# Optimization experiments

Hardware: AMD Instinct MI355X
Metric: run time of the kernel (lower is better)

The kernel has to match this reference:

```python
import jax, jax.numpy as jnp
import numpy as np
from jax import lax

DN = ('NCHW', 'OIHW', 'NCHW')
BN_EPS = 1e-5


def _conv(x, w, pad):
    # pad: list of (lo, hi) for H, W
    return lax.conv_general_dilated(x, w, (1, 1), pad, dimension_numbers=DN)


def _grid_sample_bilinear(img, grid):
    """F.grid_sample(img, grid, align_corners=True, padding_mode='zeros').
    img: [N,C,H,W], grid: [N,Ho,Wo,2] with (x,y) in [-1,1]."""
    N, C, H, W = img.shape
    gx, gy = grid[..., 0], grid[..., 1]
    # align_corners=True mapping to pixel coords
    ix = (gx + 1.0) * 0.5 * (W - 1)
    iy = (gy + 1.0) * 0.5 * (H - 1)
    x0 = jnp.floor(ix)
    y0 = jnp.floor(iy)
    x1 = x0 + 1.0
    y1 = y0 + 1.0
    # bilinear weights
    wa = (x1 - ix) * (y1 - iy)  # top-left (x0,y0)
    wb = (ix - x0) * (y1 - iy)  # top-right (x1,y0)
    wc = (x1 - ix) * (iy - y0)  # bottom-left (x0,y1)
    wd = (ix - x0) * (iy - y0)  # bottom-right (x1,y1)

    imgc = jnp.transpose(img, (0, 2, 3, 1))  # [N,H,W,C]
    b = jnp.arange(N)[:, None, None]

    def gather(xi, yi):
        valid = (xi >= 0) & (xi <= W - 1) & (yi >= 0) & (yi <= H - 1)
        xc = jnp.clip(xi, 0, W - 1).astype(jnp.int32)
        yc = jnp.clip(yi, 0, H - 1).astype(jnp.int32)
        v = imgc[b, yc, xc]  # [N,Ho,Wo,C]
        return v * valid[..., None].astype(img.dtype)

    out = (gather(x0, y0) * wa[..., None] + gather(x1, y0) * wb[..., None]
           + gather(x0, y1) * wc[..., None] + gather(x1, y1) * wd[..., None])
    return jnp.transpose(out, (0, 3, 1, 2))  # [N,C,Ho,Wo]


def setup_inputs() -> dict:
    key = jax.random.key(0)
    ks = jax.random.split(key, 12)
    N, C1, C2 = 8, 512, 256
    H, W = 64, 64
    x1 = jax.random.normal(ks[0], (N, C1, 2 * H, 2 * W), dtype=jnp.float32)
    x2 = jax.random.normal(ks[1], (N, C2, H, W), dtype=jnp.float32)
    w_change = jax.random.normal(ks[2], (C2, C1, 1, 1), dtype=jnp.float32) * 0.02
    b_change = jax.random.normal(ks[3], (C2,), dtype=jnp.float32) * 0.02
    w_cc1 = jax.random.normal(ks[4], (C2, 2 * C2, 1, 1), dtype=jnp.float32) * 0.02
    bn_gamma = 1.0 + 0.1 * jax.random.normal(ks[5], (C2,), dtype=jnp.float32)
    bn_beta = 0.1 * jax.random.normal(ks[6], (C2,), dtype=jnp.float32)
    bn_mean = 0.1 * jax.random.normal(ks[7], (C2,), dtype=jnp.float32)
    bn_var = jax.random.uniform(ks[8], (C2,), dtype=jnp.float32, minval=0.5, maxval=1.5)
    w_cc2 = jax.random.normal(ks[9], (4, C2, 3, 3), dtype=jnp.float32) * 0.02
    return {"x1": x1, "x2": x2, "w_change": w_change, "b_change": b_change,
            "w_cc1": w_cc1, "bn_gamma": bn_gamma, "bn_beta": bn_beta,
            "bn_mean": bn_mean, "bn_var": bn_var, "w_cc2": w_cc2}


def reference(x1, x2, w_change, b_change, w_cc1, bn_gamma, bn_beta, bn_mean, bn_var, w_cc2):
    # MaxPool2d(2,2)
    x1p = lax.reduce_window(x1, -jnp.inf, lax.max, (1, 1, 2, 2), (1, 1, 2, 2), 'VALID')
    # change: 1x1 conv with bias
    x1c = _conv(x1p, w_change, [(0, 0), (0, 0)]) + b_change[None, :, None, None]
    # concat + concat_conv (1x1 conv -> BN(eval) -> ReLU -> 3x3 conv)
    x = jnp.concatenate([x1c, x2], axis=1)
    x = _conv(x, w_cc1, [(0, 0), (0, 0)])
    inv = lax.rsqrt(bn_var + BN_EPS)
    x = (x - bn_mean[None, :, None, None]) * (inv * bn_gamma)[None, :, None, None] + bn_beta[None, :, None, None]
    x = jax.nn.relu(x)
    flow = _conv(x, w_cc2, [(1, 1), (1, 1)])  # [N,4,H,W]
    flow1 = flow[:, :2]
    flow2 = flow[:, 2:]

    N, _, H, W = x1c.shape
    # base grid: [...,0]=x over width, [...,1]=y over height
    xs = jnp.linspace(-1.0, 1.0, W, dtype=x1c.dtype)
    ys = jnp.linspace(-1.0, 1.0, H, dtype=x1c.dtype)
    base = jnp.stack(jnp.meshgrid(xs, ys, indexing='xy'), axis=-1)  # [H,W,2]
    norm = jnp.array([(W - 1) / 2.0, (H - 1) / 2.0], dtype=x1c.dtype)

    grid1 = base[None] + jnp.transpose(flow1, (0, 2, 3, 1)) / norm
    grid2 = base[None] + jnp.transpose(flow2, (0, 2, 3, 1)) / norm

    u1 = _grid_sample_bilinear(x1c, grid1)
    u2 = _grid_sample_bilinear(x2, grid2)
    return u1 + u2
```

## Files before the change

### kernel.cpp

```cpp
#include <hip/hip_runtime.h>
#include <hip/hip_bf16.h>

#define NB 8
#define C1 512
#define C2 256
#define HWSZ 4096
#define BN_EPS 1e-5f
#define P2 264

typedef __hip_bfloat16 bf16;
typedef __hip_bfloat162 bf162;
typedef __attribute__((ext_vector_type(8))) short short8v;
typedef __attribute__((ext_vector_type(4))) float f32x4;

static __device__ inline float b2f(bf16 h) { return __bfloat162float(h); }

static __device__ inline float us2f(unsigned short u) {
  union { unsigned u32; float f; } c; c.u32 = ((unsigned)u) << 16; return c.f;
}

static __device__ inline unsigned short f2bf(float f) {
  union { bf16 h; unsigned short u; } c;
  c.h = __float2bfloat16(f);
  return c.u;
}

static __device__ inline unsigned pack2(float a, float b) {
  union { unsigned u; bf162 h; } pk;
  pk.h = __float22bfloat162_rn(make_float2(a, b));
  return pk.u;
}

static __device__ inline uint2 pack4(float a, float b, float c, float d) {
  union { uint2 u; bf162 h[2]; } pk;
  pk.h[0] = __float22bfloat162_rn(make_float2(a, b));
  pk.h[1] = __float22bfloat162_rn(make_float2(c, d));
  return pk.u;
}

#define SBARQ() asm volatile("s_waitcnt lgkmcnt(0)\n\ts_barrier" ::: "memory")
#define SBAR()  asm volatile("s_barrier" ::: "memory")
#define LGKM0() asm volatile("s_waitcnt lgkmcnt(0)" ::: "memory")

__global__ __launch_bounds__(256) void k0_swizzle(
    const float* __restrict__ wch, const float* __restrict__ wcc1,
    const float* __restrict__ wcc2,
    unsigned short* __restrict__ wchB, unsigned short* __restrict__ wcc1B,
    float* __restrict__ wr) {
  const int t = blockIdx.x * 256 + threadIdx.x;
  if (t < 262144) {
    const int which = t >> 17;
    const int r = t & 131071;
    const int i = r & 7;
    const int lane = (r >> 3) & 63;
    const int ntile = (r >> 9) & 15;
    const int kstep = r >> 13;
    const int ci = kstep * 32 + (lane >> 4) * 8 + i;
    const int co = ntile * 16 + (lane & 15);
    const float* s = which ? wcc1 : wch;
    unsigned short* d = which ? wcc1B : wchB;
    d[r] = f2bf(s[co * 512 + ci]);
  } else if (t < 262144 + 9216) {
    const int r = t - 262144;
    const int f = r / 2304;
    const int rr = r % 2304;
    const int ci = rr / 9;
    const int tt = rr % 9;
    wr[ci * 36 + (tt / 3) * 12 + (tt % 3) * 4 + f] = wcc2[r];
  }
}

__global__ __launch_bounds__(512) void k12_fused(
    const float* __restrict__ x1, const float* __restrict__ x2,
    const unsigned short* __restrict__ wchB, const unsigned short* __restrict__ wcc1B,
    const float* __restrict__ bch,
    const float* __restrict__ gamma, const float* __restrict__ beta,
    const float* __restrict__ mean, const float* __restrict__ var,
    unsigned short* __restrict__ x1c_nhwc, unsigned short* __restrict__ x2_nhwc,
    bf16* __restrict__ xbn) {
  __shared__ unsigned short As[64 * 40];
  __shared__ unsigned short As2[64 * P2];
  const int tid = threadIdx.x;
  const int lane = tid & 63;
  const int wv = tid >> 6;
  const int lrow = lane & 15;
  const int lgrp = lane >> 4;

  const int m0g = blockIdx.x * 64;
  const int n = m0g >> 12;
  const int hw0 = m0g & 4095;
  const int h = hw0 >> 6;

  f32x4 acc[4][2];
#pragma unroll
  for (int mt = 0; mt < 4; ++mt)
#pragma unroll
    for (int nt = 0; nt < 2; ++nt) acc[mt][nt] = (f32x4){0.f, 0.f, 0.f, 0.f};

  const int pmi = tid & 31;
  const int ms = pmi * 2;
  const int ch0 = (tid >> 5) * 2;

  const float* x1p = x1 + (size_t)n * C1 * 16384 + (size_t)(2 * h) * 128 + 2 * ms;

  float4 t0, b0, t1, b1;
#define LOADA(K0_) do { \
    const float* p_ = x1p + (size_t)((K0_) + ch0) * 16384; \
    t0 = *(const float4*)p_;            b0 = *(const float4*)(p_ + 128); \
    t1 = *(const float4*)(p_ + 16384);  b1 = *(const float4*)(p_ + 16384 + 128); \
  } while (0)
#define POOLA(U0_, U1_) do { \
    U0_ = pack2(fmaxf(fmaxf(t0.x, t0.y), fmaxf(b0.x, b0.y)), \
                fmaxf(fmaxf(t1.x, t1.y), fmaxf(b1.x, b1.y))); \
    U1_ = pack2(fmaxf(fmaxf(t0.z, t0.w), fmaxf(b0.z, b0.w)), \
                fmaxf(fmaxf(t1.z, t1.w), fmaxf(b1.z, b1.w))); \
  } while (0)

  unsigned uA0, uA1;
  LOADA(0);
  POOLA(uA0, uA1);
  LOADA(32);

  for (int ks = 0; ks < 16; ++ks) {
    SBARQ();
    *(unsigned*)&As[ms * 40 + ch0] = uA0;
    *(unsigned*)&As[(ms + 1) * 40 + ch0] = uA1;
    LGKM0();
    SBAR();

    unsigned uN0, uN1;
    if (ks < 15) {
      POOLA(uN0, uN1);
      if (ks < 14) LOADA((ks + 2) * 32);
    }

    short8v a[4];
#pragma unroll
    for (int mt = 0; mt < 4; ++mt)
      a[mt] = *(const short8v*)&As[(mt * 16 + lrow) * 40 + lgrp * 8];
#pragma unroll
    for (int nt = 0; nt < 2; ++nt) {
      const int ntile = wv * 2 + nt;
      const short8v b = *(const short8v*)&wchB[(size_t)((ks * 16 + ntile) * 64 + lane) * 8];
#pragma unroll
      for (int mt = 0; mt < 4; ++mt)
        acc[mt][nt] = __builtin_amdgcn_mfma_f32_16x16x32_bf16(a[mt], b, acc[mt][nt], 0, 0, 0);
    }
    if (ks < 15) { uA0 = uN0; uA1 = uN1; }
  }

  const int chB = tid >> 4;
  const int mqB = (tid & 15) * 4;
  float4 cf0 = *(const float4*)&x2[((size_t)(n * C2 + chB)) * HWSZ + hw0 + mqB];
  float4 cf1 = *(const float4*)&x2[((size_t)(n * C2 + 32 + chB)) * HWSZ + hw0 + mqB];

#pragma unroll
  for (int nt = 0; nt < 2; ++nt) {
    const int co = (wv * 2 + nt) * 16 + lrow;
    const float bias = bch[co];
#pragma unroll
    for (int mt = 0; mt < 4; ++mt) {
      const f32x4 v = acc[mt][nt];
      const uint2 pk = pack4(v.x + bias, v.y + bias, v.z + bias, v.w + bias);
      const int mb = mt * 16 + lgrp * 4;
      As2[(mb + 0) * P2 + co] = (unsigned short)(pk.x & 0xffffu);
      As2[(mb + 1) * P2 + co] = (unsigned short)(pk.x >> 16);
      As2[(mb + 2) * P2 + co] = (unsigned short)(pk.y & 0xffffu);
      As2[(mb + 3) * P2 + co] = (unsigned short)(pk.y >> 16);
      acc[mt][nt] = (f32x4){0.f, 0.f, 0.f, 0.f};
    }
  }
  LGKM0();
  SBAR();

  {
    const int mm = tid >> 3;
    const int cg = (tid & 7) * 32;
    const size_t ob = ((size_t)(m0g + mm)) * 256 + cg;
#pragma unroll
    for (int k = 0; k < 4; ++k) {
      const uint4 v = *(const uint4*)&As2[mm * P2 + cg + k * 8];
      *(uint4*)&x1c_nhwc[ob + k * 8] = v;
    }
  }

#pragma unroll
  for (int ks = 0; ks < 8; ++ks) {
    short8v a[4];
#pragma unroll
    for (int mt = 0; mt < 4; ++mt)
      a[mt] = *(const short8v*)&As2[(mt * 16 + lrow) * P2 + ks * 32 + lgrp * 8];
#pragma unroll
    for (int nt = 0; nt < 2; ++nt) {
      const int ntile = wv * 2 + nt;
      const short8v b = *(const short8v*)&wcc1B[(size_t)((ks * 16 + ntile) * 64 + lane) * 8];
#pragma unroll
      for (int mt = 0; mt < 4; ++mt)
        acc[mt][nt] = __builtin_amdgcn_mfma_f32_16x16x32_bf16(a[mt], b, acc[mt][nt], 0, 0, 0);
    }
  }

  for (int ks = 8; ks < 16; ++ks) {
    const unsigned p0 = pack2(cf0.x, cf0.y);
    const unsigned p1 = pack2(cf0.z, cf0.w);
    cf0 = cf1;
    if (ks < 14) {
      cf1 = *(const float4*)&x2[((size_t)(n * C2 + (ks - 6) * 32 + chB)) * HWSZ + hw0 + mqB];
    }
    SBARQ();
    As[(mqB + 0) * 40 + chB] = (unsigned short)(p0 & 0xffffu);
    As[(mqB + 1) * 40 + chB] = (unsigned short)(p0 >> 16);
    As[(mqB + 2) * 40 + chB] = (unsigned short)(p1 & 0xffffu);
    As[(mqB + 3) * 40 + chB] = (unsigned short)(p1 >> 16);
    LGKM0();
    SBAR();

    {
      const int m = tid >> 3;
      const int c4 = (tid & 7) * 4;
      const uint2 v = *(const uint2*)&As[m * 40 + c4];
      *(uint2*)&x2_nhwc[((size_t)(m0g + m)) * 256 + (ks - 8) * 32 + c4] = v;
    }

    short8v a[4];
#pragma unroll
    for (int mt = 0; mt < 4; ++mt)
      a[mt] = *(const short8v*)&As[(mt * 16 + lrow) * 40 + lgrp * 8];
#pragma unroll
    for (int nt = 0; nt < 2; ++nt) {
      const int ntile = wv * 2 + nt;
      const short8v b = *(const short8v*)&wcc1B[(size_t)((ks * 16 + ntile) * 64 + lane) * 8];
#pragma unroll
      for (int mt = 0; mt < 4; ++mt)
        acc[mt][nt] = __builtin_amdgcn_mfma_f32_16x16x32_bf16(a[mt], b, acc[mt][nt], 0, 0, 0);
    }
  }

#pragma unroll
  for (int nt = 0; nt < 2; ++nt) {
    const int co = (wv * 2 + nt) * 16 + lrow;
    const float sc = gamma[co] * rsqrtf(var[co] + BN_EPS);
    const float sh = beta[co] - mean[co] * sc;
#pragma unroll
    for (int mt = 0; mt < 4; ++mt) {
      const f32x4 vv = acc[mt][nt];
      *(uint2*)&xbn[((size_t)(n * C2 + co)) * HWSZ + hw0 + mt * 16 + lgrp * 4] =
          pack4(fmaxf(vv.x * sc + sh, 0.f), fmaxf(vv.y * sc + sh, 0.f),
                fmaxf(vv.z * sc + sh, 0.f), fmaxf(vv.w * sc + sh, 0.f));
    }
  }
#undef LOADA
#undef POOLA
}

__global__ __launch_bounds__(1024) void k34_conv_sample(
    const bf16* __restrict__ xbn, const float* __restrict__ wr,
    const unsigned short* __restrict__ x1c_nhwc,
    const unsigned short* __restrict__ x2_nhwc,
    float* __restrict__ out) {
  __shared__ union {
    struct { float wsm[9216]; float part[16][4][64]; } c;
    float outT[256][65];
  } sh;
  __shared__ float flr[4][64];
  __shared__ int   toff[8][64];
  __shared__ float twt[8][64];

  const int tid = threadIdx.x;
  const int n = blockIdx.x >> 6;
  const int h = blockIdx.x & 63;
  const int wl = tid & 63;
  const int q = tid >> 6;

  for (int idx = tid; idx < 9216; idx += 1024) sh.c.wsm[idx] = wr[idx];
  __syncthreads();

  float acc[4] = {0.f, 0.f, 0.f, 0.f};
  {
    const bf16* base = xbn + ((size_t)(n * C2 + q * 16)) * HWSZ;
    const float* wq = sh.c.wsm + (q * 16) * 36;
    for (int cc = 0; cc < 16; ++cc) {
      const bf16* src = base + (size_t)cc * HWSZ;
      const float* wc = wq + cc * 36;
#pragma unroll
      for (int dy = 0; dy < 3; ++dy) {
        const int y = h + dy - 1;
        if ((unsigned)y >= 64u) continue;
        const float v = b2f(src[y * 64 + wl]);
        float vm = __shfl_up(v, 1);
        float vp = __shfl_down(v, 1);
        if (wl == 0) vm = 0.f;
        if (wl == 63) vp = 0.f;
        const float4 wa = *(const float4*)&wc[dy * 12 + 0];
        const float4 wb = *(const float4*)&wc[dy * 12 + 4];
        const float4 wd = *(const float4*)&wc[dy * 12 + 8];
        acc[0] = fmaf(vm, wa.x, fmaf(v, wb.x, fmaf(vp, wd.x, acc[0])));
        acc[1] = fmaf(vm, wa.y, fmaf(v, wb.y, fmaf(vp, wd.y, acc[1])));
        acc[2] = fmaf(vm, wa.z, fmaf(v, wb.z, fmaf(vp, wd.z, acc[2])));
        acc[3] = fmaf(vm, wa.w, fmaf(v, wb.w, fmaf(vp, wd.w, acc[3])));
      }
    }
  }
  sh.c.part[q][0][wl] = acc[0];
  sh.c.part[q][1][wl] = acc[1];
  sh.c.part[q][2][wl] = acc[2];
  sh.c.part[q][3][wl] = acc[3];
  __syncthreads();
  if (tid < 256) {
    const int f = tid >> 6;
    const int ww = tid & 63;
    float s = 0.f;
#pragma unroll
    for (int qq = 0; qq < 16; ++qq) s += sh.c.part[qq][f][ww];
    flr[f][ww] = s;
  }
  __syncthreads();

  if (tid < 64) {
    const float fxv[2] = {flr[0][tid], flr[2][tid]};
    const float fyv[2] = {flr[1][tid], flr[3][tid]};
#pragma unroll
    for (int s = 0; s < 2; ++s) {
      const float ix = (float)tid + fxv[s], iy = (float)h + fyv[s];
      const float x0f = floorf(ix), y0f = floorf(iy);
      const float fx = ix - x0f, fy = iy - y0f;
      const int x0 = (int)x0f, y0 = (int)y0f, x1i = x0 + 1, y1i = y0 + 1;
      const float vx0 = (x0 >= 0 && x0 < 64) ? 1.f : 0.f;
      const float vx1 = (x1i >= 0 && x1i < 64) ? 1.f : 0.f;
      const float vy0 = (y0 >= 0 && y0 < 64) ? 1.f : 0.f;
      const float vy1 = (y1i >= 0 && y1i < 64) ? 1.f : 0.f;
      const int cx0 = min(max(x0, 0), 63), cx1 = min(max(x1i, 0), 63);
      const int cy0 = min(max(y0, 0), 63), cy1 = min(max(y1i, 0), 63);
      toff[s * 4 + 0][tid] = cy0 * 64 + cx0;
      toff[s * 4 + 1][tid] = cy0 * 64 + cx1;
      toff[s * 4 + 2][tid] = cy1 * 64 + cx0;
      toff[s * 4 + 3][tid] = cy1 * 64 + cx1;
      twt[s * 4 + 0][tid] = (1.f - fx) * (1.f - fy) * vx0 * vy0;
      twt[s * 4 + 1][tid] = fx * (1.f - fy) * vx1 * vy0;
      twt[s * 4 + 2][tid] = (1.f - fx) * fy * vx0 * vy1;
      twt[s * 4 + 3][tid] = fx * fy * vx1 * vy1;
    }
  }
  __syncthreads();

  {
    const unsigned short* pb1 = x1c_nhwc + (size_t)n * HWSZ * 256 + wl * 4;
    const unsigned short* pb2 = x2_nhwc + (size_t)n * HWSZ * 256 + wl * 4;
#pragma unroll
    for (int pp = 0; pp < 4; ++pp) {
      const int p = q * 4 + pp;
      float u0 = 0.f, u1 = 0.f, u2 = 0.f, u3 = 0.f;
#pragma unroll
      for (int t = 0; t < 8; ++t) {
        const int off = toff[t][p];
        const float wt = twt[t][p];
        const unsigned short* rp = (t < 4 ? pb1 : pb2) + (size_t)off * 256;
        const uint2 v = *(const uint2*)rp;
        u0 = fmaf(wt, us2f((unsigned short)(v.x & 0xffffu)), u0);
        u1 = fmaf(wt, us2f((unsigned short)(v.x >> 16)), u1);
        u2 = fmaf(wt, us2f((unsigned short)(v.y & 0xffffu)), u2);
        u3 = fmaf(wt, us2f((unsigned short)(v.y >> 16)), u3);
      }
      sh.outT[wl * 4 + 0][p] = u0;
      sh.outT[wl * 4 + 1][p] = u1;
      sh.outT[wl * 4 + 2][p] = u2;
      sh.outT[wl * 4 + 3][p] = u3;
    }
  }
  __syncthreads();

  {
    const int p = tid & 63;
    const int cg = (tid >> 6) * 16;
    const size_t ob = ((size_t)(n * C2 + cg)) * HWSZ + h * 64 + p;
#pragma unroll
    for (int j = 0; j < 16; ++j) {
      out[ob + (size_t)j * HWSZ] = sh.outT[cg + j][p];
    }
  }
}

extern "C" void kernel_launch(void* const* d_in, const int* in_sizes, int n_in,
                              void* d_out, int out_size, void* d_ws, size_t ws_size,
                              hipStream_t stream) {
  const float* x1      = (const float*)d_in[0];
  const float* x2      = (const float*)d_in[1];
  const float* w_change= (const float*)d_in[2];
  const float* b_change= (const float*)d_in[3];
  const float* w_cc1   = (const float*)d_in[4];
  const float* bn_gamma= (const float*)d_in[5];
  const float* bn_beta = (const float*)d_in[6];
  const float* bn_mean = (const float*)d_in[7];
  const float* bn_var  = (const float*)d_in[8];
  const float* w_cc2   = (const float*)d_in[9];
  float* out = (float*)d_out;

  unsigned short* x1c_nhwc = (unsigned short*)d_ws;
  bf16*           xbn      = (bf16*)((char*)d_ws + (16u << 20));
  unsigned short* x2_nhwc  = (unsigned short*)((char*)d_ws + (32u << 20));
  unsigned short* wchB     = (unsigned short*)((char*)d_ws + (48u << 20));
  unsigned short* wcc1B    = (unsigned short*)((char*)d_ws + (48u << 20) + (256u << 10));
  float*          wr       = (float*)((char*)d_ws + (48u << 20) + (512u << 10));

  k0_swizzle<<<1060, 256, 0, stream>>>(w_change, w_cc1, w_cc2, wchB, wcc1B, wr);
  k12_fused<<<512, 512, 0, stream>>>(x1, x2, wchB, wcc1B, b_change,
                                     bn_gamma, bn_beta, bn_mean, bn_var,
                                     x1c_nhwc, x2_nhwc, xbn);
  k34_conv_sample<<<512, 1024, 0, stream>>>(xbn, wr, x1c_nhwc, x2_nhwc, out);
}
```

Before: 139.5 us.

## Fuse 3x3 flow conv into 1x1 conv kernel via shared-memory staging and atomics

The BN+ReLU output is now kept in shared memory inside the fused 1x1-conv kernel instead of being written to global memory as bf16. The same kernel computes the 3x3 flow convolution for its row and scatters partial sums to the neighbouring rows of a zero-initialized flow buffer with atomicAdd. The sampling kernel then only reads the precomputed flow. This removes a 16 MB intermediate write and read and the weight staging in the last kernel. In exchange it adds float atomics, which make the summation order nondeterministic, and an extra zeroing pass in the prep kernel.

```diff
diff --git a/kernel.cpp b/kernel.cpp
--- a/kernel.cpp
+++ b/kernel.cpp
@@ -13,8 +13,6 @@
 typedef __attribute__((ext_vector_type(8))) short short8v;
 typedef __attribute__((ext_vector_type(4))) float f32x4;
 
-static __device__ inline float b2f(bf16 h) { return __bfloat162float(h); }
-
 static __device__ inline float us2f(unsigned short u) {
   union { unsigned u32; float f; } c; c.u32 = ((unsigned)u) << 16; return c.f;
 }
@@ -42,11 +40,11 @@
 #define SBAR()  asm volatile("s_barrier" ::: "memory")
 #define LGKM0() asm volatile("s_waitcnt lgkmcnt(0)" ::: "memory")
 
-__global__ __launch_bounds__(256) void k0_swizzle(
+__global__ __launch_bounds__(256) void k0_prep(
     const float* __restrict__ wch, const float* __restrict__ wcc1,
     const float* __restrict__ wcc2,
     unsigned short* __restrict__ wchB, unsigned short* __restrict__ wcc1B,
-    float* __restrict__ wr) {
+    float* __restrict__ wr, float* __restrict__ flow) {
   const int t = blockIdx.x * 256 + threadIdx.x;
   if (t < 262144) {
     const int which = t >> 17;
@@ -67,6 +65,8 @@
     const int ci = rr / 9;
     const int tt = rr % 9;
     wr[ci * 36 + (tt / 3) * 12 + (tt % 3) * 4 + f] = wcc2[r];
+  } else if (t < 262144 + 9216 + 131072) {
+    flow[t - 262144 - 9216] = 0.f;
   }
 }
 
@@ -76,8 +76,9 @@
     const float* __restrict__ bch,
     const float* __restrict__ gamma, const float* __restrict__ beta,
     const float* __restrict__ mean, const float* __restrict__ var,
+    const float* __restrict__ wr,
     unsigned short* __restrict__ x1c_nhwc, unsigned short* __restrict__ x2_nhwc,
-    bf16* __restrict__ xbn) {
+    float* __restrict__ flow) {
   __shared__ unsigned short As[64 * 40];
   __shared__ unsigned short As2[64 * P2];
   const int tid = threadIdx.x;
@@ -236,6 +237,7 @@
     }
   }
 
+  SBARQ();
 #pragma unroll
   for (int nt = 0; nt < 2; ++nt) {
     const int co = (wv * 2 + nt) * 16 + lrow;
@@ -244,24 +246,55 @@
 #pragma unroll
     for (int mt = 0; mt < 4; ++mt) {
       const f32x4 vv = acc[mt][nt];
-      *(uint2*)&xbn[((size_t)(n * C2 + co)) * HWSZ + hw0 + mt * 16 + lgrp * 4] =
-          pack4(fmaxf(vv.x * sc + sh, 0.f), fmaxf(vv.y * sc + sh, 0.f),
-                fmaxf(vv.z * sc + sh, 0.f), fmaxf(vv.w * sc + sh, 0.f));
-    }
+      const uint2 pk = pack4(fmaxf(vv.x * sc + sh, 0.f), fmaxf(vv.y * sc + sh, 0.f),
+                             fmaxf(vv.z * sc + sh, 0.f), fmaxf(vv.w * sc + sh, 0.f));
+      const int mb = mt * 16 + lgrp * 4;
+      As2[(mb + 0) * P2 + co] = (unsigned short)(pk.x & 0xffffu);
+      As2[(mb + 1) * P2 + co] = (unsigned short)(pk.x >> 16);
+      As2[(mb + 2) * P2 + co] = (unsigned short)(pk.y & 0xffffu);
+      As2[(mb + 3) * P2 + co] = (unsigned short)(pk.y >> 16);
+    }
+  }
+  LGKM0();
+  SBAR();
+
+  {
+    const int xp = tid & 63;
+    const int fh = tid >> 6;
+    const int f = fh & 3;
+    const int half = fh >> 2;
+    float pm = 0.f, pz = 0.f, pp = 0.f;
+    for (int ci = half * 128; ci < half * 128 + 128; ci += 2) {
+      const float* w0 = wr + ci * 36 + f;
+#pragma unroll
+      for (int dx = 0; dx < 3; ++dx) {
+        const int xs = xp + dx - 1;
+        if ((unsigned)xs >= 64u) continue;
+        const unsigned vv = *(const unsigned*)&As2[xs * P2 + ci];
+        const float v0 = us2f((unsigned short)(vv & 0xffffu));
+        const float v1 = us2f((unsigned short)(vv >> 16));
+        const float* wa = w0 + dx * 4;
+        const float* wb = wa + 36;
+        pm = fmaf(v0, wa[24], fmaf(v1, wb[24], pm));
+        pz = fmaf(v0, wa[12], fmaf(v1, wb[12], pz));
+        pp = fmaf(v0, wa[0],  fmaf(v1, wb[0],  pp));
+      }
+    }
+    float* fb = flow + ((size_t)(n * 4 + f)) * HWSZ + xp;
+    if (h >= 1)  atomicAdd(fb + (h - 1) * 64, pm);
+    atomicAdd(fb + h * 64, pz);
+    if (h <= 62) atomicAdd(fb + (h + 1) * 64, pp);
   }
 #undef LOADA
 #undef POOLA
 }
 
-__global__ __launch_bounds__(1024) void k34_conv_sample(
-    const bf16* __restrict__ xbn, const float* __restrict__ wr,
+__global__ __launch_bounds__(1024) void k4_sample(
+    const float* __restrict__ flow,
     const unsigned short* __restrict__ x1c_nhwc,
     const unsigned short* __restrict__ x2_nhwc,
     float* __restrict__ out) {
-  __shared__ union {
-    struct { float wsm[9216]; float part[16][4][64]; } c;
-    float outT[256][65];
-  } sh;
+  __shared__ float outT[256][65];
   __shared__ float flr[4][64];
   __shared__ int   toff[8][64];
   __shared__ float twt[8][64];
@@ -272,47 +305,9 @@
   const int wl = tid & 63;
   const int q = tid >> 6;
 
-  for (int idx = tid; idx < 9216; idx += 1024) sh.c.wsm[idx] = wr[idx];
-  __syncthreads();
-
-  float acc[4] = {0.f, 0.f, 0.f, 0.f};
-  {
-    const bf16* base = xbn + ((size_t)(n * C2 + q * 16)) * HWSZ;
-    const float* wq = sh.c.wsm + (q * 16) * 36;
-    for (int cc = 0; cc < 16; ++cc) {
-      const bf16* src = base + (size_t)cc * HWSZ;
-      const float* wc = wq + cc * 36;
-#pragma unroll
-      for (int dy = 0; dy < 3; ++dy) {
-        const int y = h + dy - 1;
-        if ((unsigned)y >= 64u) continue;
-        const float v = b2f(src[y * 64 + wl]);
-        float vm = __shfl_up(v, 1);
-        float vp = __shfl_down(v, 1);
-        if (wl == 0) vm = 0.f;
-        if (wl == 63) vp = 0.f;
-        const float4 wa = *(const float4*)&wc[dy * 12 + 0];
-        const float4 wb = *(const float4*)&wc[dy * 12 + 4];
-        const float4 wd = *(const float4*)&wc[dy * 12 + 8];
-        acc[0] = fmaf(vm, wa.x, fmaf(v, wb.x, fmaf(vp, wd.x, acc[0])));
-        acc[1] = fmaf(vm, wa.y, fmaf(v, wb.y, fmaf(vp, wd.y, acc[1])));
-        acc[2] = fmaf(vm, wa.z, fmaf(v, wb.z, fmaf(vp, wd.z, acc[2])));
-        acc[3] = fmaf(vm, wa.w, fmaf(v, wb.w, fmaf(vp, wd.w, acc[3])));
-      }
-    }
-  }
-  sh.c.part[q][0][wl] = acc[0];
-  sh.c.part[q][1][wl] = acc[1];
-  sh.c.part[q][2][wl] = acc[2];
-  sh.c.part[q][3][wl] = acc[3];
-  __syncthreads();
   if (tid < 256) {
-    const int f = tid >> 6;
-    const int ww = tid & 63;
-    float s = 0.f;
-#pragma unroll
-    for (int qq = 0; qq < 16; ++qq) s += sh.c.part[qq][f][ww];
-    flr[f][ww] = s;
+    flr[tid >> 6][tid & 63] =
+        flow[((size_t)(n * 4 + (tid >> 6))) * HWSZ + h * 64 + (tid & 63)];
   }
   __syncthreads();
 
@@ -361,10 +356,10 @@
         u2 = fmaf(wt, us2f((unsigned short)(v.y & 0xffffu)), u2);
         u3 = fmaf(wt, us2f((unsigned short)(v.y >> 16)), u3);
       }
-      sh.outT[wl * 4 + 0][p] = u0;
-      sh.outT[wl * 4 + 1][p] = u1;
-      sh.outT[wl * 4 + 2][p] = u2;
-      sh.outT[wl * 4 + 3][p] = u3;
+      outT[wl * 4 + 0][p] = u0;
+      outT[wl * 4 + 1][p] = u1;
+      outT[wl * 4 + 2][p] = u2;
+      outT[wl * 4 + 3][p] = u3;
     }
   }
   __syncthreads();
@@ -375,7 +370,7 @@
     const size_t ob = ((size_t)(n * C2 + cg)) * HWSZ + h * 64 + p;
 #pragma unroll
     for (int j = 0; j < 16; ++j) {
-      out[ob + (size_t)j * HWSZ] = sh.outT[cg + j][p];
+      out[ob + (size_t)j * HWSZ] = outT[cg + j][p];
     }
   }
 }
@@ -396,15 +391,15 @@
   float* out = (float*)d_out;
 
   unsigned short* x1c_nhwc = (unsigned short*)d_ws;
-  bf16*           xbn      = (bf16*)((char*)d_ws + (16u << 20));
-  unsigned short* x2_nhwc  = (unsigned short*)((char*)d_ws + (32u << 20));
-  unsigned short* wchB     = (unsigned short*)((char*)d_ws + (48u << 20));
-  unsigned short* wcc1B    = (unsigned short*)((char*)d_ws + (48u << 20) + (256u << 10));
-  float*          wr       = (float*)((char*)d_ws + (48u << 20) + (512u << 10));
-
-  k0_swizzle<<<1060, 256, 0, stream>>>(w_change, w_cc1, w_cc2, wchB, wcc1B, wr);
+  unsigned short* x2_nhwc  = (unsigned short*)((char*)d_ws + (16u << 20));
+  float*          flow     = (float*)((char*)d_ws + (32u << 20));
+  unsigned short* wchB     = (unsigned short*)((char*)d_ws + (32u << 20) + (512u << 10));
+  unsigned short* wcc1B    = (unsigned short*)((char*)d_ws + (32u << 20) + (768u << 10));
+  float*          wr       = (float*)((char*)d_ws + (33u << 20));
+
+  k0_prep<<<1572, 256, 0, stream>>>(w_change, w_cc1, w_cc2, wchB, wcc1B, wr, flow);
   k12_fused<<<512, 512, 0, stream>>>(x1, x2, wchB, wcc1B, b_change,
-                                     bn_gamma, bn_beta, bn_mean, bn_var,
-                                     x1c_nhwc, x2_nhwc, xbn);
-  k34_conv_sample<<<512, 1024, 0, stream>>>(xbn, wr, x1c_nhwc, x2_nhwc, out);
-}
+                                     bn_gamma, bn_beta, bn_mean, bn_var, wr,
+                                     x1c_nhwc, x2_nhwc, flow);
+  k4_sample<<<512, 1024, 0, stream>>>(flow, x1c_nhwc, x2_nhwc, out);
+}
```

After: 140.4 us. No clear change (+0.6%).
